# Performance work log

Measured on AMD Instinct MI355X. Metric: run time of the kernel, lower is better.

The kernel has to match this reference:

```python
import jax, jax.numpy as jnp
import numpy as np

B, N, IN_C, OUT_C, H, M, E = 1, 20000, 256, 64, 4, 30, 320000
EPS = 1e-6


def _projection_matrix(m, d, seed=0):
    # NodeFormer create_projection_matrix: stacked transposed-QR blocks, rows
    # rescaled by norms of iid gaussian rows (scaling=0).
    rng = np.random.RandomState(seed)
    blocks = []
    nb_full = m // d
    for _ in range(nb_full):
        q, _ = np.linalg.qr(rng.randn(d, d))
        blocks.append(q.T)
    rem = m - nb_full * d
    if rem > 0:
        q, _ = np.linalg.qr(rng.randn(d, d))
        blocks.append(q.T[:rem])
    final = np.vstack(blocks)
    multiplier = np.linalg.norm(rng.randn(m, d), axis=1)
    return jnp.asarray(multiplier[:, None] * final, dtype=jnp.float32)


def _linear(key, out_f, in_f):
    k1, k2 = jax.random.split(key)
    s = 1.0 / np.sqrt(in_f)
    w = jax.random.uniform(k1, (out_f, in_f), jnp.float32, -s, s)
    b = jax.random.uniform(k2, (out_f,), jnp.float32, -s, s)
    return w, b


def setup_inputs() -> dict:
    key = jax.random.key(0)
    ks = jax.random.split(key, 8)
    Wq_w, Wq_b = _linear(ks[3], H * OUT_C, IN_C)
    Wk_w, Wk_b = _linear(ks[4], H * OUT_C, IN_C)
    Wv_w, Wv_b = _linear(ks[5], H * OUT_C, IN_C)
    Wo_w, Wo_b = _linear(ks[6], OUT_C, H * OUT_C)
    return {
        'z': jax.random.normal(ks[0], (B, N, IN_C), jnp.float32),
        'feat': jax.random.normal(ks[1], (B, N, IN_C), jnp.float32),
        'edge_index': jax.random.randint(ks[2], (2, E), 0, N),
        'tau': jnp.asarray(0.25, jnp.float32),
        'Wq_w': Wq_w, 'Wq_b': Wq_b,
        'Wk_w': Wk_w, 'Wk_b': Wk_b,
        'Wv_w': Wv_w, 'Wv_b': Wv_b,
        'Wo_w': Wo_w, 'Wo_b': Wo_b,
        'b_param': jnp.full((1, H), 0.1, jnp.float32),  # rb_order=1, sigmoid init
        'proj': _projection_matrix(M, OUT_C),
    }


def _softmax_kernel(x, proj, is_query):
    # Performer positive softmax kernel feature map. x: [B,N,H,D] -> [B,N,H,M]
    d = x.shape[-1]
    x = x * (float(d) ** -0.25)
    ratio = 1.0 / jnp.sqrt(jnp.asarray(proj.shape[0], x.dtype))
    xd = jnp.einsum('bnhd,md->bnhm', x, proj)
    diag = 0.5 * jnp.sum(x * x, axis=-1, keepdims=True)
    if is_query:
        mx = jnp.max(xd, axis=-1, keepdims=True)
    else:
        mx = jnp.max(jnp.max(xd, axis=-1, keepdims=True), axis=1, keepdims=True)
    return ratio * (jnp.exp(xd - diag - mx) + EPS)


def reference(z, feat, edge_index, tau, Wq_w, Wq_b, Wk_w, Wk_b, Wv_w, Wv_b,
              Wo_w, Wo_b, b_param, proj):
    Bn, Nn = z.shape[0], z.shape[1]
    q = (feat @ Wq_w.T + Wq_b).reshape(Bn, Nn, H, OUT_C)
    k = (feat @ Wk_w.T + Wk_b).reshape(Bn, Nn, H, OUT_C)
    v = (z @ Wv_w.T + Wv_b).reshape(Bn, Nn, H, OUT_C)

    inv = 1.0 / jnp.sqrt(tau)
    qp = _softmax_kernel(q * inv, proj, True)    # [B,N,H,M]
    kp = _softmax_kernel(k * inv, proj, False)   # [B,N,H,M]

    # Linear (kernelized) attention, O(N*H*M*D)
    kvs = jnp.einsum('bnhm,bnhd->bhmd', kp, v)
    num = jnp.einsum('bnhm,bhmd->bnhd', qp, kvs)
    den = jnp.einsum('bnhm,bhm->bnh', qp, jnp.sum(kp, axis=1))[..., None]
    z_next = num / den                            # [B,N,H,D]

    # Relational bias: GCN-style normalized scatter with per-head scalar weight
    row, col = edge_index[0], edge_index[1]
    d_in = jnp.zeros((Nn,), z.dtype).at[col].add(1.0)
    d_out = jnp.zeros((Nn,), z.dtype).at[row].add(1.0)
    edge_w = jnp.nan_to_num(jnp.sqrt(1.0 / d_in[col]) * jnp.sqrt(1.0 / d_out[row]),
                            nan=0.0, posinf=0.0, neginf=0.0)    # [E]
    msgs = v[:, row] * edge_w[None, :, None, None]              # [B,E,H,D]
    agg = jnp.zeros_like(v).at[:, col].add(msgs)                # [B,N,H,D]
    z_next = z_next + jax.nn.sigmoid(b_param[0])[None, None, :, None] * agg

    out = z_next.reshape(Bn, Nn, H * OUT_C) @ Wo_w.T + Wo_b     # [B,N,OUT_C]
    return out
```

## Files before the change

kernel.cpp:

```cpp
#include <hip/hip_runtime.h>

#define NN 20000
#define EE 320000
#define RATIO_F 0.18257418583505536f
#define EPS_F 1e-6f
#define SCALE_D4 0.35355339059327373f
#define NCH 157

typedef _Float16 f16x8 __attribute__((ext_vector_type(8)));
typedef _Float16 f16x4 __attribute__((ext_vector_type(4)));
typedef float f32x4 __attribute__((ext_vector_type(4)));

__device__ __forceinline__ unsigned fenc(float x) {
  unsigned u = __float_as_uint(x);
  return (u & 0x80000000u) ? ~u : (u | 0x80000000u);
}
__device__ __forceinline__ float fdec(unsigned u) {
  return (u & 0x80000000u) ? __uint_as_float(u & 0x7FFFFFFFu) : __uint_as_float(~u);
}
__device__ __forceinline__ void fma4(float* a, float s, float4 b) {
  a[0] = fmaf(s, b.x, a[0]);
  a[1] = fmaf(s, b.y, a[1]);
  a[2] = fmaf(s, b.z, a[2]);
  a[3] = fmaf(s, b.w, a[3]);
}
__device__ __forceinline__ void gload16(const void* g, void* l) {
  __builtin_amdgcn_global_load_lds(
      (const __attribute__((address_space(1))) unsigned int*)g,
      (__attribute__((address_space(3))) unsigned int*)l, 16, 0, 0);
}

__global__ __launch_bounds__(256)
void k0_build(const float* __restrict__ Wq, const float* __restrict__ Wk,
              const float* __restrict__ Wv, const float* __restrict__ bq,
              const float* __restrict__ bk, const float* __restrict__ bv,
              const float* __restrict__ proj, const float* __restrict__ tau,
              const float* __restrict__ Wo, const int* __restrict__ ei,
              const float* __restrict__ feat, const float* __restrict__ zin,
              _Float16* __restrict__ Wf, float* __restrict__ bbig,
              _Float16* __restrict__ WoFh, _Float16* __restrict__ WoFl,
              int* __restrict__ dini, int* __restrict__ douti,
              _Float16* __restrict__ feath, _Float16* __restrict__ zh16) {
  const int blk = blockIdx.x;
  const int i = threadIdx.x;
  if (blk >= 1401) {
    int cb = blk - 1401;
    const float* src;
    _Float16* dst;
    if (cb < 2500) { src = feat; dst = feath; }
    else           { src = zin;  dst = zh16; cb -= 2500; }
    const size_t off = (size_t)cb * 2048 + i * 8;
    const float4 a = *(const float4*)(src + off);
    const float4 b = *(const float4*)(src + off + 4);
    f16x8 o;
    o[0] = (_Float16)a.x; o[1] = (_Float16)a.y;
    o[2] = (_Float16)a.z; o[3] = (_Float16)a.w;
    o[4] = (_Float16)b.x; o[5] = (_Float16)b.y;
    o[6] = (_Float16)b.z; o[7] = (_Float16)b.w;
    *(f16x8*)(dst + off) = o;
    return;
  }
  if (blk >= 1088) {
    const int q = (blk - 1088) * 256 + i;
    if (q < EE / 4) {
      const int4 r4 = *(const int4*)(ei + q * 4);
      const int4 c4 = *(const int4*)(ei + EE + q * 4);
      atomicAdd(&dini[c4.x], 1); atomicAdd(&dini[c4.y], 1);
      atomicAdd(&dini[c4.z], 1); atomicAdd(&dini[c4.w], 1);
      atomicAdd(&douti[r4.x], 1); atomicAdd(&douti[r4.y], 1);
      atomicAdd(&douti[r4.z], 1); atomicAdd(&douti[r4.w], 1);
    }
    return;
  }
  const int kt = i >> 5, gg = (i >> 3) & 3, j = i & 7;
  if (blk >= 1024) {
    const int col = blk - 1024;
    const float val = Wo[col * 256 + i];
    const int lane = gg * 16 + (col & 15);
    const size_t off = (size_t)((col >> 4) * 8 + kt) * 512 + lane * 8 + j;
    const _Float16 hb = (_Float16)val;
    WoFh[off] = hb;
    WoFl[off] = (_Float16)(val - (float)hb);
    return;
  }
  const int col = blk;
  const float s = rsqrtf(tau[0]) * SCALE_D4;
  float val = 0.f, bias = 0.f;
  if (col < 256) {
    val = Wq[col * 256 + i]; bias = bq[col];
  } else if (col < 512) {
    const int c = col - 256;
    val = Wk[c * 256 + i]; bias = bk[c];
  } else if (col < 768) {
    const int c = col - 512;
    val = Wv[c * 256 + i]; bias = bv[c];
  } else {
    const int rr = col - 768;
    const int grp = rr >> 7;
    const int h = (rr >> 5) & 3, m = rr & 31;
    if (m < 30) {
      const float* W = grp ? Wk : Wq;
      const float* bb = grp ? bk : bq;
      float a = 0.f, ba = 0.f;
#pragma unroll 8
      for (int d = 0; d < 64; ++d) {
        const float pr = proj[m * 64 + d];
        a  = fmaf(pr, W[(h * 64 + d) * 256 + i], a);
        ba = fmaf(pr, bb[h * 64 + d], ba);
      }
      val = s * a; bias = s * ba;
    }
  }
  const int lane = gg * 16 + (col & 15);
  const size_t off = (size_t)((col >> 4) * 8 + kt) * 512 + lane * 8 + j;
  Wf[off] = (_Float16)val;
  if (i == 0) bbig[col] = bias;
}

__device__ __forceinline__ int ct_of(int s, int isv, int h, int y) {
  if (isv) return 32 + (y - 4) * 8 + s;
  if (s < 4)  return h * 4 + s;
  if (s < 8)  return 16 + h * 4 + (s - 4);
  if (s < 10) return 48 + 2 * h + (s - 8);
  return 56 + 2 * h + (s - 10);
}

__global__ __launch_bounds__(512, 4)
void k1_all(const _Float16* __restrict__ feath, const _Float16* __restrict__ zh16,
            const _Float16* __restrict__ Wf, const float* __restrict__ bbig,
            const float* __restrict__ tau,
            _Float16* __restrict__ qph, float* __restrict__ kbuf,
            _Float16* __restrict__ vh, unsigned* __restrict__ kmaxU) {
  __shared__ __align__(16) _Float16 blds[12 * 2048];
  const int t = threadIdx.x;
  const int wid = t >> 6, lane = t & 63;
  const int g = lane >> 4, cl = lane & 15;
  const int y = blockIdx.y;
  const int h = y & 3;
  const int rbase = blockIdx.x * 128 + wid * 16;
  int arow = rbase + cl; if (arow > NN - 1) arow = NN - 1;

  if (y < 4) {
    const _Float16* arp = feath + (size_t)arow * 256;
#pragma unroll
    for (int r = 0; r < 6; ++r) {
      const int idx = r * 4096 + t * 8;
      const int s = idx >> 11, wi = idx & 2047;
      gload16(Wf + (size_t)ct_of(s, 0, h, y) * 4096 + wi, &blds[idx]);
    }
    f16x8 Ah[4];
#pragma unroll
    for (int l = 0; l < 4; ++l)
      Ah[l] = *(const f16x8*)(arp + l * 32 + g * 8);
    __syncthreads();
    f16x8 Ah2[4];
#pragma unroll
    for (int l = 0; l < 4; ++l)
      Ah2[l] = *(const f16x8*)(arp + (l + 4) * 32 + g * 8);
    f32x4 acc[12];
#pragma unroll
    for (int s = 0; s < 12; ++s) acc[s] = (f32x4){0.f, 0.f, 0.f, 0.f};
#pragma unroll
    for (int ktl = 0; ktl < 4; ++ktl) {
#pragma unroll
      for (int s = 0; s < 12; ++s) {
        const f16x8 b = *(const f16x8*)&blds[s * 2048 + ktl * 512 + lane * 8];
        acc[s] = __builtin_amdgcn_mfma_f32_16x16x32_f16(Ah[ktl], b, acc[s], 0, 0, 0);
      }
    }
    __syncthreads();
#pragma unroll
    for (int r = 0; r < 6; ++r) {
      const int idx = r * 4096 + t * 8;
      const int s = idx >> 11, wi = idx & 2047;
      gload16(Wf + (size_t)ct_of(s, 0, h, y) * 4096 + 2048 + wi, &blds[idx]);
    }
    __syncthreads();
#pragma unroll
    for (int ktl = 0; ktl < 4; ++ktl) {
#pragma unroll
      for (int s = 0; s < 12; ++s) {
        const f16x8 b = *(const f16x8*)&blds[s * 2048 + ktl * 512 + lane * 8];
        acc[s] = __builtin_amdgcn_mfma_f32_16x16x32_f16(Ah2[ktl], b, acc[s], 0, 0, 0);
      }
    }
#pragma unroll
    for (int s = 0; s < 12; ++s) {
      const float bb = bbig[ct_of(s, 0, h, y) * 16 + cl];
#pragma unroll
      for (int j = 0; j < 4; ++j) acc[s][j] += bb;
    }
    const float sc = rsqrtf(tau[0]) * SCALE_D4;
    const float h2 = 0.5f * sc * sc;
    float dsq[4], dsk[4];
#pragma unroll
    for (int j = 0; j < 4; ++j) {
      dsq[j] = acc[0][j] * acc[0][j] + acc[1][j] * acc[1][j] +
               acc[2][j] * acc[2][j] + acc[3][j] * acc[3][j];
      dsk[j] = acc[4][j] * acc[4][j] + acc[5][j] * acc[5][j] +
               acc[6][j] * acc[6][j] + acc[7][j] * acc[7][j];
    }
#pragma unroll
    for (int m = 1; m < 16; m <<= 1) {
#pragma unroll
      for (int j = 0; j < 4; ++j) {
        dsq[j] += __shfl_xor(dsq[j], m);
        dsk[j] += __shfl_xor(dsk[j], m);
      }
    }
    {
#pragma unroll
      for (int j = 0; j < 4; ++j) {
        const float x0 = acc[8][j], x1 = acc[9][j];
        float mv = fmaxf(x0, (cl < 14) ? x1 : -3.4e38f);
#pragma unroll
        for (int m = 1; m < 16; m <<= 1) mv = fmaxf(mv, __shfl_xor(mv, m));
        const float dg = h2 * dsq[j];
        const int r = rbase + 4 * g + j;
        if (r < NN) {
          _Float16* dst = qph + (size_t)r * 120 + h * 30;
          dst[cl] = (_Float16)(RATIO_F * (expf(x0 - dg - mv) + EPS_F));
          if (cl < 14)
            dst[16 + cl] = (_Float16)(RATIO_F * (expf(x1 - dg - mv) + EPS_F));
        }
      }
    }
    {
      float wmax = -3.4e38f;
#pragma unroll
      for (int j = 0; j < 4; ++j) {
        const float x0 = acc[10][j], x1 = acc[11][j];
        float mv = fmaxf(x0, (cl < 14) ? x1 : -3.4e38f);
#pragma unroll
        for (int m = 1; m < 16; m <<= 1) mv = fmaxf(mv, __shfl_xor(mv, m));
        wmax = fmaxf(wmax, mv);
        const float dg = h2 * dsk[j];
        const int r = rbase + 4 * g + j;
        if (r < NN) {
          float* dst = kbuf + (size_t)r * 120 + h * 30;
          dst[cl] = x0 - dg;
          if (cl < 14) dst[16 + cl] = x1 - dg;
        }
      }
      wmax = fmaxf(wmax, __shfl_xor(wmax, 16));
      wmax = fmaxf(wmax, __shfl_xor(wmax, 32));
      if (lane == 0) atomicMax(&kmaxU[h], fenc(wmax));
    }
  } else {
    const _Float16* arp = zh16 + (size_t)arow * 256;
#pragma unroll
    for (int r = 0; r < 4; ++r) {
      const int idx = r * 4096 + t * 8;
      const int s = idx >> 11, wi = idx & 2047;
      gload16(Wf + (size_t)ct_of(s, 1, h, y) * 4096 + wi, &blds[idx]);
    }
    f16x8 Ah[4];
#pragma unroll
    for (int l = 0; l < 4; ++l)
      Ah[l] = *(const f16x8*)(arp + l * 32 + g * 8);
    __syncthreads();
    f16x8 Ah2[4];
#pragma unroll
    for (int l = 0; l < 4; ++l)
      Ah2[l] = *(const f16x8*)(arp + (l + 4) * 32 + g * 8);
    f32x4 acc[8];
#pragma unroll
    for (int s = 0; s < 8; ++s) acc[s] = (f32x4){0.f, 0.f, 0.f, 0.f};
#pragma unroll
    for (int ktl = 0; ktl < 4; ++ktl) {
#pragma unroll
      for (int s = 0; s < 8; ++s) {
        const f16x8 b = *(const f16x8*)&blds[s * 2048 + ktl * 512 + lane * 8];
        acc[s] = __builtin_amdgcn_mfma_f32_16x16x32_f16(Ah[ktl], b, acc[s], 0, 0, 0);
      }
    }
    __syncthreads();
#pragma unroll
    for (int r = 0; r < 4; ++r) {
      const int idx = r * 4096 + t * 8;
      const int s = idx >> 11, wi = idx & 2047;
      gload16(Wf + (size_t)ct_of(s, 1, h, y) * 4096 + 2048 + wi, &blds[idx]);
    }
    __syncthreads();
#pragma unroll
    for (int ktl = 0; ktl < 4; ++ktl) {
#pragma unroll
      for (int s = 0; s < 8; ++s) {
        const f16x8 b = *(const f16x8*)&blds[s * 2048 + ktl * 512 + lane * 8];
        acc[s] = __builtin_amdgcn_mfma_f32_16x16x32_f16(Ah2[ktl], b, acc[s], 0, 0, 0);
      }
    }
#pragma unroll
    for (int s = 0; s < 8; ++s) {
      const int ct = ct_of(s, 1, h, y);
      const float bb = bbig[ct * 16 + cl];
      const int colb = (ct - 32) * 16 + cl;
#pragma unroll
      for (int j = 0; j < 4; ++j) {
        const int r = rbase + 4 * g + j;
        if (r < NN) vh[(size_t)r * 256 + colb] = (_Float16)(acc[s][j] + bb);
      }
    }
  }
}

__global__ __launch_bounds__(256)
void k3_kvs(const float* __restrict__ kbr, const _Float16* __restrict__ vh,
            const unsigned* __restrict__ kmaxU, float* __restrict__ partial) {
  __shared__ float kpch[128 * 32];
  __shared__ float vch[128 * 68];
  const int h = blockIdx.y;
  const int n0 = blockIdx.x * 128;
  const int cnt = min(128, NN - n0);
  const int t = threadIdx.x;
  const float mx = fdec(kmaxU[h]);
  const int m = t >> 3, dg = t & 7, d0 = dg * 8;
#pragma unroll
  for (int l = 0; l < 15; ++l) {
    const int flat = l * 256 + t;
    const int nl = flat / 30, mm = flat - nl * 30;
    kpch[nl * 32 + mm] = (nl < cnt)
        ? RATIO_F * (expf(kbr[(size_t)(n0 + nl) * 120 + h * 30 + mm] - mx) + EPS_F)
        : 0.f;
  }
#pragma unroll
  for (int l = 0; l < 8; ++l) {
    const int f4 = l * 256 + t;
    const int nl = f4 >> 4, dd = (f4 & 15) * 4;
    float4 vv = make_float4(0.f, 0.f, 0.f, 0.f);
    if (nl < cnt) {
      f16x4 u = *(const f16x4*)(vh + (size_t)(n0 + nl) * 256 + h * 64 + dd);
      vv = make_float4((float)u[0], (float)u[1], (float)u[2], (float)u[3]);
    }
    *(float4*)&vch[nl * 68 + dd] = vv;
  }
  __syncthreads();
  float acc[8] = {0, 0, 0, 0, 0, 0, 0, 0};
  float asum = 0.f;
  const int ms = (m < 30) ? m : 0;
  for (int nl = 0; nl < cnt; ++nl) {
    const float kv = kpch[nl * 32 + ms];
    const float4 va = *(const float4*)&vch[nl * 68 + d0];
    const float4 vb = *(const float4*)&vch[nl * 68 + d0 + 4];
    fma4(&acc[0], kv, va);
    fma4(&acc[4], kv, vb);
    asum += kv;
  }
  if (m < 30) {
    float* dst = partial + ((size_t)blockIdx.y * NCH + blockIdx.x) * 1952 + m * 64 + d0;
#pragma unroll
    for (int j = 0; j < 8; ++j) dst[j] = acc[j];
    if (dg == 0)
      partial[((size_t)blockIdx.y * NCH + blockIdx.x) * 1952 + 1920 + m] = asum;
  }
}

__global__ __launch_bounds__(256)
void k3b_reduce(const float* __restrict__ partial, float* __restrict__ kvs,
                float* __restrict__ ksum) {
  const int idx = blockIdx.x * 256 + threadIdx.x;
  if (idx >= 4 * 1952) return;
  const int h = idx / 1952, q = idx - h * 1952;
  float s = 0.f;
  for (int c = 0; c < NCH; ++c)
    s += partial[((size_t)h * NCH + c) * 1952 + q];
  if (q < 1920) kvs[h * 1920 + q] = s;
  else if (q < 1950) ksum[h * 30 + (q - 1920)] = s;
}

__global__ __launch_bounds__(256)
void k4_attn(const _Float16* __restrict__ qph, const float* __restrict__ kvs,
             const float* __restrict__ ksum, const _Float16* __restrict__ aggh,
             const float* __restrict__ bp, _Float16* __restrict__ zh) {
  __shared__ float kvsl[120 * 68];
  __shared__ float ksl[120];
  __shared__ float qpl[32 * 120];
  const int t = threadIdx.x;
  const int n0 = blockIdx.x * 32;
#pragma unroll
  for (int l = 0; l < 30; ++l) {
    const int f = l * 256 + t;
    const int hm = f >> 6, d = f & 63;
    kvsl[hm * 68 + d] = kvs[f];
  }
  if (t < 120) ksl[t] = ksum[t];
#pragma unroll
  for (int l = 0; l < 15; ++l) {
    const int f = l * 256 + t;
    qpl[f] = (float)qph[(size_t)n0 * 120 + f];
  }
  __syncthreads();
  const int nl = t >> 3, dg = t & 7, d0 = dg * 8;
  const float* qrow = &qpl[nl * 120];
  float den[4] = {0, 0, 0, 0};
  for (int m = 0; m < 30; ++m) {
#pragma unroll
    for (int hh = 0; hh < 4; ++hh) den[hh] = fmaf(qrow[hh * 30 + m], ksl[hh * 30 + m], den[hh]);
  }
  float acc[4][8] = {};
  for (int m = 0; m < 30; ++m) {
#pragma unroll
    for (int hh = 0; hh < 4; ++hh) {
      const float qv = qrow[hh * 30 + m];
      const float* kr = &kvsl[(hh * 30 + m) * 68 + d0];
      const float4 ka = *(const float4*)kr;
      const float4 kb = *(const float4*)(kr + 4);
      fma4(&acc[hh][0], qv, ka);
      fma4(&acc[hh][4], qv, kb);
    }
  }
  const size_t n = n0 + nl;
#pragma unroll
  for (int hh = 0; hh < 4; ++hh) {
    const float inv = 1.0f / den[hh];
    const float sg = 1.f / (1.f + expf(-bp[hh]));
    const f16x8 ag = *(const f16x8*)(aggh + n * 256 + hh * 64 + d0);
    f16x8 o;
#pragma unroll
    for (int jj = 0; jj < 8; ++jj)
      o[jj] = (_Float16)(acc[hh][jj] * inv + sg * (float)ag[jj]);
    *(f16x8*)(zh + n * 256 + hh * 64 + d0) = o;
  }
}

__global__ __launch_bounds__(1024)
void k6a_scan(const int* __restrict__ cnt, int* __restrict__ off) {
  __shared__ int s[1024];
  const int t = threadIdx.x;
  int4 v[5];
  int sum = 0;
  const int4* p4 = (const int4*)(cnt + t * 20);
#pragma unroll
  for (int i = 0; i < 5; ++i) {
    v[i] = p4[i];
    sum += v[i].x + v[i].y + v[i].z + v[i].w;
  }
  s[t] = sum;
  __syncthreads();
  for (int o = 1; o < 1024; o <<= 1) {
    const int add = (t >= o) ? s[t - o] : 0;
    __syncthreads();
    s[t] += add;
    __syncthreads();
  }
  int run = (t == 0) ? 0 : s[t - 1];
  if (t == 0) off[0] = 0;
  const int base = t * 20;
#pragma unroll
  for (int i = 0; i < 5; ++i) {
    const int vals[4] = {v[i].x, v[i].y, v[i].z, v[i].w};
#pragma unroll
    for (int j = 0; j < 4; ++j) {
      const int idx = base + i * 4 + j;
      if (idx < NN) { run += vals[j]; off[idx + 1] = run; }
    }
  }
}

__global__ __launch_bounds__(256)
void k6bc(const int* __restrict__ ei, const int* __restrict__ coff,
          int* __restrict__ cursor, int* __restrict__ crow,
          const int* __restrict__ douti, float* __restrict__ rw) {
  const int b = blockIdx.x;
  if (b < EE / 256) {
    const int e = b * 256 + threadIdx.x;
    const int r = ei[e], c = ei[EE + e];
    const int pos = atomicAdd(&cursor[c], 1);
    crow[coff[c] + pos] = r;
  } else {
    const int n = (b - EE / 256) * 256 + threadIdx.x;
    if (n < NN) rw[n] = rsqrtf((float)douti[n]);
  }
}

__global__ __launch_bounds__(256)
void k7g_gather(const int* __restrict__ coff, const int* __restrict__ crow,
                const float* __restrict__ rw, const _Float16* __restrict__ vh,
                _Float16* __restrict__ aggh) {
  const int node = blockIdx.x * 4 + (threadIdx.x >> 6);
  const int lane = threadIdx.x & 63;
  const int o0 = coff[node], o1 = coff[node + 1];
  float a0 = 0.f, a1 = 0.f, a2 = 0.f, a3 = 0.f;
  if (o1 > o0) {
    int e = o0;
    for (; e + 16 <= o1; e += 16) {
      int rr[16];
#pragma unroll
      for (int u = 0; u < 16; ++u) rr[u] = crow[e + u];
      float ww[16];
#pragma unroll
      for (int u = 0; u < 16; ++u) ww[u] = rw[rr[u]];
#pragma unroll
      for (int u = 0; u < 16; ++u) {
        const f16x4 vv = *(const f16x4*)(vh + (size_t)rr[u] * 256 + lane * 4);
        a0 = fmaf(ww[u], (float)vv[0], a0);
        a1 = fmaf(ww[u], (float)vv[1], a1);
        a2 = fmaf(ww[u], (float)vv[2], a2);
        a3 = fmaf(ww[u], (float)vv[3], a3);
      }
    }
    for (; e + 4 <= o1; e += 4) {
      int rr[4];
#pragma unroll
      for (int u = 0; u < 4; ++u) rr[u] = crow[e + u];
      float ww[4];
#pragma unroll
      for (int u = 0; u < 4; ++u) ww[u] = rw[rr[u]];
#pragma unroll
      for (int u = 0; u < 4; ++u) {
        const f16x4 vv = *(const f16x4*)(vh + (size_t)rr[u] * 256 + lane * 4);
        a0 = fmaf(ww[u], (float)vv[0], a0);
        a1 = fmaf(ww[u], (float)vv[1], a1);
        a2 = fmaf(ww[u], (float)vv[2], a2);
        a3 = fmaf(ww[u], (float)vv[3], a3);
      }
    }
    for (; e < o1; ++e) {
      const int r = crow[e];
      const float wr = rw[r];
      const f16x4 vv = *(const f16x4*)(vh + (size_t)r * 256 + lane * 4);
      a0 = fmaf(wr, (float)vv[0], a0);
      a1 = fmaf(wr, (float)vv[1], a1);
      a2 = fmaf(wr, (float)vv[2], a2);
      a3 = fmaf(wr, (float)vv[3], a3);
    }
    const float rin = rsqrtf((float)(o1 - o0));
    a0 *= rin; a1 *= rin; a2 *= rin; a3 *= rin;
  }
  f16x4 st;
  st[0] = (_Float16)a0; st[1] = (_Float16)a1;
  st[2] = (_Float16)a2; st[3] = (_Float16)a3;
  *(f16x4*)(aggh + (size_t)node * 256 + lane * 4) = st;
}

__global__ __launch_bounds__(512, 4)
void k8m_out(const _Float16* __restrict__ zh, const _Float16* __restrict__ WoFh,
             const _Float16* __restrict__ WoFl, const float* __restrict__ bo,
             float* __restrict__ out) {
  __shared__ __align__(16) _Float16 blds[8 * 4096];
  const int t = threadIdx.x;
  const int wid = t >> 6, lane = t & 63;
  const int g = lane >> 4, cl = lane & 15;
  const int rt = wid >> 2, ct = wid & 3;
  const int rbase = blockIdx.x * 32 + rt * 16;
  int arow = rbase + cl; if (arow > NN - 1) arow = NN - 1;
#pragma unroll
  for (int s = 0; s < 4; ++s) {
    gload16(WoFh + (size_t)s * 4096 + t * 8, &blds[(s * 512 + t) * 8]);
    gload16(WoFl + (size_t)s * 4096 + t * 8, &blds[((s + 4) * 512 + t) * 8]);
  }
  const _Float16* zr = zh + (size_t)arow * 256;
  f16x8 Ah[8];
#pragma unroll
  for (int kt = 0; kt < 8; ++kt)
    Ah[kt] = *(const f16x8*)(zr + kt * 32 + g * 8);
  __syncthreads();
  f32x4 acc = {0.f, 0.f, 0.f, 0.f};
#pragma unroll
  for (int kt = 0; kt < 8; ++kt) {
    const f16x8 bh = *(const f16x8*)&blds[ct * 4096 + kt * 512 + lane * 8];
    const f16x8 bl = *(const f16x8*)&blds[(ct + 4) * 4096 + kt * 512 + lane * 8];
    acc = __builtin_amdgcn_mfma_f32_16x16x32_f16(Ah[kt], bh, acc, 0, 0, 0);
    acc = __builtin_amdgcn_mfma_f32_16x16x32_f16(Ah[kt], bl, acc, 0, 0, 0);
  }
  const float bb = bo[ct * 16 + cl];
#pragma unroll
  for (int j = 0; j < 4; ++j) {
    const int r = rbase + 4 * g + j;
    if (r < NN) out[(size_t)r * 64 + ct * 16 + cl] = acc[j] + bb;
  }
}

extern "C" void kernel_launch(void* const* d_in, const int* in_sizes, int n_in,
                              void* d_out, int out_size, void* d_ws, size_t ws_size,
                              hipStream_t stream) {
  (void)in_sizes; (void)n_in; (void)out_size; (void)ws_size;
  const float* z    = (const float*)d_in[0];
  const float* feat = (const float*)d_in[1];
  const int*   ei   = (const int*)d_in[2];
  const float* tau  = (const float*)d_in[3];
  const float* Wq_w = (const float*)d_in[4];
  const float* Wq_b = (const float*)d_in[5];
  const float* Wk_w = (const float*)d_in[6];
  const float* Wk_b = (const float*)d_in[7];
  const float* Wv_w = (const float*)d_in[8];
  const float* Wv_b = (const float*)d_in[9];
  const float* Wo_w = (const float*)d_in[10];
  const float* Wo_b = (const float*)d_in[11];
  const float* bp   = (const float*)d_in[12];
  const float* proj = (const float*)d_in[13];
  float* out = (float*)d_out;

  char* p = (char*)d_ws;
  auto alloc = [&](size_t bytes) { char* r = p; p += (bytes + 255) & ~(size_t)255; return r; };
  _Float16* Wf    = (_Float16*)alloc((size_t)256 * 1024 * 2);
  _Float16* WoFh  = (_Float16*)alloc((size_t)64 * 256 * 2);
  _Float16* WoFl  = (_Float16*)alloc((size_t)64 * 256 * 2);
  float*    bbig  = (float*)alloc(1024 * 4);
  _Float16* feath = (_Float16*)alloc((size_t)NN * 256 * 2);
  _Float16* zh16  = (_Float16*)alloc((size_t)NN * 256 * 2);
  _Float16* vh    = (_Float16*)alloc((size_t)NN * 256 * 2);
  _Float16* aggh  = (_Float16*)alloc((size_t)NN * 256 * 2);
  _Float16* qph   = (_Float16*)alloc((size_t)NN * 120 * 2);
  float*    kbuf  = (float*)alloc((size_t)NN * 120 * 4);
  _Float16* zh    = (_Float16*)alloc((size_t)NN * 256 * 2);
  float*    partial = (float*)alloc((size_t)4 * NCH * 1952 * 4);
  float*    kvs   = (float*)alloc(7680 * 4);
  float*    ksum  = (float*)alloc(120 * 4);
  float*    rw    = (float*)alloc((size_t)NN * 4);
  char* z0 = p;
  unsigned* kmaxU = (unsigned*)alloc(16);
  int*      dini  = (int*)alloc((size_t)20480 * 4);
  int*      douti = (int*)alloc((size_t)NN * 4);
  int*      cursor= (int*)alloc((size_t)NN * 4);
  char* z1 = p;
  int*      coff  = (int*)alloc((size_t)(NN + 1) * 4);
  int*      crow  = (int*)alloc((size_t)EE * 4);

  hipMemsetAsync(z0, 0, (size_t)(z1 - z0), stream);

  k0_build<<<1401 + 5000, 256, 0, stream>>>(
      Wq_w, Wk_w, Wv_w, Wq_b, Wk_b, Wv_b, proj, tau, Wo_w, ei, feat, z,
      Wf, bbig, WoFh, WoFl, dini, douti, feath, zh16);
  k6a_scan<<<1, 1024, 0, stream>>>(dini, coff);
  k6bc<<<EE / 256 + (NN + 255) / 256, 256, 0, stream>>>(ei, coff, cursor, crow,
                                                        douti, rw);
  k1_all<<<dim3(157, 6), 512, 0, stream>>>(feath, zh16, Wf, bbig, tau, qph, kbuf, vh, kmaxU);
  k7g_gather<<<NN / 4, 256, 0, stream>>>(coff, crow, rw, vh, aggh);
  k3_kvs<<<dim3(NCH, 4), 256, 0, stream>>>(kbuf, vh, kmaxU, partial);
  k3b_reduce<<<(4 * 1952 + 255) / 256, 256, 0, stream>>>(partial, kvs, ksum);
  k4_attn<<<NN / 32, 256, 0, stream>>>(qph, kvs, ksum, aggh, bp, zh);
  k8m_out<<<628, 512, 0, stream>>>(zh, WoFh, WoFl, Wo_b, out);
}
```

Before: 254.5 us.

## Merge CSR fill into projection kernel, fuse gather with kvs reduce, store k logits in fp16

The CSR row fill and degree-weight kernel is folded into the projection kernel as extra blocks, and the edge gather is merged with the kvs partial reduction into one launch. Two kernel launches go away and the independent work can overlap. The key logits buffer is now stored as fp16 instead of fp32, which halves its write and read traffic but loses precision before the exp. Merging the CSR fill into the projection grid also changes the dependency: before the gather, only block-level ordering within one launch exists, so the fill and gather are still kept in separate kernels.

```diff
diff --git a/kernel.cpp b/kernel.cpp
--- a/kernel.cpp
+++ b/kernel.cpp
@@ -126,18 +126,34 @@
 }
 
 __global__ __launch_bounds__(512, 4)
-void k1_all(const _Float16* __restrict__ feath, const _Float16* __restrict__ zh16,
-            const _Float16* __restrict__ Wf, const float* __restrict__ bbig,
-            const float* __restrict__ tau,
-            _Float16* __restrict__ qph, float* __restrict__ kbuf,
-            _Float16* __restrict__ vh, unsigned* __restrict__ kmaxU) {
+void k1m(const _Float16* __restrict__ feath, const _Float16* __restrict__ zh16,
+         const _Float16* __restrict__ Wf, const float* __restrict__ bbig,
+         const float* __restrict__ tau,
+         _Float16* __restrict__ qph, _Float16* __restrict__ kbufh,
+         _Float16* __restrict__ vh, unsigned* __restrict__ kmaxU,
+         const int* __restrict__ ei, const int* __restrict__ coff,
+         int* __restrict__ cursor, int* __restrict__ crow,
+         const int* __restrict__ douti, float* __restrict__ rw) {
   __shared__ __align__(16) _Float16 blds[12 * 2048];
+  const int blk = blockIdx.x;
   const int t = threadIdx.x;
+  if (blk >= 1567) {
+    const int n = (blk - 1567) * 512 + t;
+    if (n < NN) rw[n] = rsqrtf((float)douti[n]);
+    return;
+  }
+  if (blk >= 942) {
+    const int e = (blk - 942) * 512 + t;
+    const int r = ei[e], c = ei[EE + e];
+    const int pos = atomicAdd(&cursor[c], 1);
+    crow[coff[c] + pos] = r;
+    return;
+  }
+  const int y = blk / 157;
+  const int h = y & 3;
   const int wid = t >> 6, lane = t & 63;
   const int g = lane >> 4, cl = lane & 15;
-  const int y = blockIdx.y;
-  const int h = y & 3;
-  const int rbase = blockIdx.x * 128 + wid * 16;
+  const int rbase = (blk - y * 157) * 128 + wid * 16;
   int arow = rbase + cl; if (arow > NN - 1) arow = NN - 1;
 
   if (y < 4) {
@@ -237,9 +253,9 @@
         const float dg = h2 * dsk[j];
         const int r = rbase + 4 * g + j;
         if (r < NN) {
-          float* dst = kbuf + (size_t)r * 120 + h * 30;
-          dst[cl] = x0 - dg;
-          if (cl < 14) dst[16 + cl] = x1 - dg;
+          _Float16* dst = kbufh + (size_t)r * 120 + h * 30;
+          dst[cl] = (_Float16)(x0 - dg);
+          if (cl < 14) dst[16 + cl] = (_Float16)(x1 - dg);
         }
       }
       wmax = fmaxf(wmax, __shfl_xor(wmax, 16));
@@ -305,7 +321,7 @@
 }
 
 __global__ __launch_bounds__(256)
-void k3_kvs(const float* __restrict__ kbr, const _Float16* __restrict__ vh,
+void k3_kvs(const _Float16* __restrict__ kbr, const _Float16* __restrict__ vh,
             const unsigned* __restrict__ kmaxU, float* __restrict__ partial) {
   __shared__ float kpch[128 * 32];
   __shared__ float vch[128 * 68];
@@ -320,7 +336,7 @@
     const int flat = l * 256 + t;
     const int nl = flat / 30, mm = flat - nl * 30;
     kpch[nl * 32 + mm] = (nl < cnt)
-        ? RATIO_F * (expf(kbr[(size_t)(n0 + nl) * 120 + h * 30 + mm] - mx) + EPS_F)
+        ? RATIO_F * (expf((float)kbr[(size_t)(n0 + nl) * 120 + h * 30 + mm] - mx) + EPS_F)
         : 0.f;
   }
 #pragma unroll
@@ -356,16 +372,76 @@
 }
 
 __global__ __launch_bounds__(256)
-void k3b_reduce(const float* __restrict__ partial, float* __restrict__ kvs,
-                float* __restrict__ ksum) {
-  const int idx = blockIdx.x * 256 + threadIdx.x;
-  if (idx >= 4 * 1952) return;
-  const int h = idx / 1952, q = idx - h * 1952;
-  float s = 0.f;
-  for (int c = 0; c < NCH; ++c)
-    s += partial[((size_t)h * NCH + c) * 1952 + q];
-  if (q < 1920) kvs[h * 1920 + q] = s;
-  else if (q < 1950) ksum[h * 30 + (q - 1920)] = s;
+void k7g3b(const int* __restrict__ coff, const int* __restrict__ crow,
+           const float* __restrict__ rw, const _Float16* __restrict__ vh,
+           _Float16* __restrict__ aggh, const float* __restrict__ partial,
+           float* __restrict__ kvs, float* __restrict__ ksum) {
+  const int blk = blockIdx.x;
+  if (blk >= 5000) {
+    const int idx = (blk - 5000) * 256 + threadIdx.x;
+    if (idx >= 4 * 1952) return;
+    const int h = idx / 1952, q = idx - h * 1952;
+    float s = 0.f;
+    for (int c = 0; c < NCH; ++c)
+      s += partial[((size_t)h * NCH + c) * 1952 + q];
+    if (q < 1920) kvs[h * 1920 + q] = s;
+    else if (q < 1950) ksum[h * 30 + (q - 1920)] = s;
+    return;
+  }
+  const int node = blk * 4 + (threadIdx.x >> 6);
+  const int lane = threadIdx.x & 63;
+  const int o0 = coff[node], o1 = coff[node + 1];
+  float a0 = 0.f, a1 = 0.f, a2 = 0.f, a3 = 0.f;
+  if (o1 > o0) {
+    int e = o0;
+    for (; e + 16 <= o1; e += 16) {
+      int rr[16];
+#pragma unroll
+      for (int u = 0; u < 16; ++u) rr[u] = crow[e + u];
+      float ww[16];
+#pragma unroll
+      for (int u = 0; u < 16; ++u) ww[u] = rw[rr[u]];
+#pragma unroll
+      for (int u = 0; u < 16; ++u) {
+        const f16x4 vv = *(const f16x4*)(vh + (size_t)rr[u] * 256 + lane * 4);
+        a0 = fmaf(ww[u], (float)vv[0], a0);
+        a1 = fmaf(ww[u], (float)vv[1], a1);
+        a2 = fmaf(ww[u], (float)vv[2], a2);
+        a3 = fmaf(ww[u], (float)vv[3], a3);
+      }
+    }
+    for (; e + 4 <= o1; e += 4) {
+      int rr[4];
+#pragma unroll
+      for (int u = 0; u < 4; ++u) rr[u] = crow[e + u];
+      float ww[4];
+#pragma unroll
+      for (int u = 0; u < 4; ++u) ww[u] = rw[rr[u]];
+#pragma unroll
+      for (int u = 0; u < 4; ++u) {
+        const f16x4 vv = *(const f16x4*)(vh + (size_t)rr[u] * 256 + lane * 4);
+        a0 = fmaf(ww[u], (float)vv[0], a0);
+        a1 = fmaf(ww[u], (float)vv[1], a1);
+        a2 = fmaf(ww[u], (float)vv[2], a2);
+        a3 = fmaf(ww[u], (float)vv[3], a3);
+      }
+    }
+    for (; e < o1; ++e) {
+      const int r = crow[e];
+      const float wr = rw[r];
+      const f16x4 vv = *(const f16x4*)(vh + (size_t)r * 256 + lane * 4);
+      a0 = fmaf(wr, (float)vv[0], a0);
+      a1 = fmaf(wr, (float)vv[1], a1);
+      a2 = fmaf(wr, (float)vv[2], a2);
+      a3 = fmaf(wr, (float)vv[3], a3);
+    }
+    const float rin = rsqrtf((float)(o1 - o0));
+    a0 *= rin; a1 *= rin; a2 *= rin; a3 *= rin;
+  }
+  f16x4 st;
+  st[0] = (_Float16)a0; st[1] = (_Float16)a1;
+  st[2] = (_Float16)a2; st[3] = (_Float16)a3;
+  *(f16x4*)(aggh + (size_t)node * 256 + lane * 4) = st;
 }
 
 __global__ __launch_bounds__(256)
@@ -455,82 +531,6 @@
       if (idx < NN) { run += vals[j]; off[idx + 1] = run; }
     }
   }
-}
-
-__global__ __launch_bounds__(256)
-void k6bc(const int* __restrict__ ei, const int* __restrict__ coff,
-          int* __restrict__ cursor, int* __restrict__ crow,
-          const int* __restrict__ douti, float* __restrict__ rw) {
-  const int b = blockIdx.x;
-  if (b < EE / 256) {
-    const int e = b * 256 + threadIdx.x;
-    const int r = ei[e], c = ei[EE + e];
-    const int pos = atomicAdd(&cursor[c], 1);
-    crow[coff[c] + pos] = r;
-  } else {
-    const int n = (b - EE / 256) * 256 + threadIdx.x;
-    if (n < NN) rw[n] = rsqrtf((float)douti[n]);
-  }
-}
-
-__global__ __launch_bounds__(256)
-void k7g_gather(const int* __restrict__ coff, const int* __restrict__ crow,
-                const float* __restrict__ rw, const _Float16* __restrict__ vh,
-                _Float16* __restrict__ aggh) {
-  const int node = blockIdx.x * 4 + (threadIdx.x >> 6);
-  const int lane = threadIdx.x & 63;
-  const int o0 = coff[node], o1 = coff[node + 1];
-  float a0 = 0.f, a1 = 0.f, a2 = 0.f, a3 = 0.f;
-  if (o1 > o0) {
-    int e = o0;
-    for (; e + 16 <= o1; e += 16) {
-      int rr[16];
-#pragma unroll
-      for (int u = 0; u < 16; ++u) rr[u] = crow[e + u];
-      float ww[16];
-#pragma unroll
-      for (int u = 0; u < 16; ++u) ww[u] = rw[rr[u]];
-#pragma unroll
-      for (int u = 0; u < 16; ++u) {
-        const f16x4 vv = *(const f16x4*)(vh + (size_t)rr[u] * 256 + lane * 4);
-        a0 = fmaf(ww[u], (float)vv[0], a0);
-        a1 = fmaf(ww[u], (float)vv[1], a1);
-        a2 = fmaf(ww[u], (float)vv[2], a2);
-        a3 = fmaf(ww[u], (float)vv[3], a3);
-      }
-    }
-    for (; e + 4 <= o1; e += 4) {
-      int rr[4];
-#pragma unroll
-      for (int u = 0; u < 4; ++u) rr[u] = crow[e + u];
-      float ww[4];
-#pragma unroll
-      for (int u = 0; u < 4; ++u) ww[u] = rw[rr[u]];
-#pragma unroll
-      for (int u = 0; u < 4; ++u) {
-        const f16x4 vv = *(const f16x4*)(vh + (size_t)rr[u] * 256 + lane * 4);
-        a0 = fmaf(ww[u], (float)vv[0], a0);
-        a1 = fmaf(ww[u], (float)vv[1], a1);
-        a2 = fmaf(ww[u], (float)vv[2], a2);
-        a3 = fmaf(ww[u], (float)vv[3], a3);
-      }
-    }
-    for (; e < o1; ++e) {
-      const int r = crow[e];
-      const float wr = rw[r];
-      const f16x4 vv = *(const f16x4*)(vh + (size_t)r * 256 + lane * 4);
-      a0 = fmaf(wr, (float)vv[0], a0);
-      a1 = fmaf(wr, (float)vv[1], a1);
-      a2 = fmaf(wr, (float)vv[2], a2);
-      a3 = fmaf(wr, (float)vv[3], a3);
-    }
-    const float rin = rsqrtf((float)(o1 - o0));
-    a0 *= rin; a1 *= rin; a2 *= rin; a3 *= rin;
-  }
-  f16x4 st;
-  st[0] = (_Float16)a0; st[1] = (_Float16)a1;
-  st[2] = (_Float16)a2; st[3] = (_Float16)a3;
-  *(f16x4*)(aggh + (size_t)node * 256 + lane * 4) = st;
 }
 
 __global__ __launch_bounds__(512, 4)
@@ -602,7 +602,7 @@
   _Float16* vh    = (_Float16*)alloc((size_t)NN * 256 * 2);
   _Float16* aggh  = (_Float16*)alloc((size_t)NN * 256 * 2);
   _Float16* qph   = (_Float16*)alloc((size_t)NN * 120 * 2);
-  float*    kbuf  = (float*)alloc((size_t)NN * 120 * 4);
+  _Float16* kbufh = (_Float16*)alloc((size_t)NN * 120 * 2);
   _Float16* zh    = (_Float16*)alloc((size_t)NN * 256 * 2);
   float*    partial = (float*)alloc((size_t)4 * NCH * 1952 * 4);
   float*    kvs   = (float*)alloc(7680 * 4);
@@ -623,12 +623,11 @@
       Wq_w, Wk_w, Wv_w, Wq_b, Wk_b, Wv_b, proj, tau, Wo_w, ei, feat, z,
       Wf, bbig, WoFh, WoFl, dini, douti, feath, zh16);
   k6a_scan<<<1, 1024, 0, stream>>>(dini, coff);
-  k6bc<<<EE / 256 + (NN + 255) / 256, 256, 0, stream>>>(ei, coff, cursor, crow,
-                                                        douti, rw);
-  k1_all<<<dim3(157, 6), 512, 0, stream>>>(feath, zh16, Wf, bbig, tau, qph, kbuf, vh, kmaxU);
-  k7g_gather<<<NN / 4, 256, 0, stream>>>(coff, crow, rw, vh, aggh);
-  k3_kvs<<<dim3(NCH, 4), 256, 0, stream>>>(kbuf, vh, kmaxU, partial);
-  k3b_reduce<<<(4 * 1952 + 255) / 256, 256, 0, stream>>>(partial, kvs, ksum);
+  k1m<<<1607, 512, 0, stream>>>(feath, zh16, Wf, bbig, tau, qph, kbufh, vh,
+                                kmaxU, ei, coff, cursor, crow, douti, rw);
+  k3_kvs<<<dim3(NCH, 4), 256, 0, stream>>>(kbufh, vh, kmaxU, partial);
+  k7g3b<<<5000 + (4 * 1952 + 255) / 256, 256, 0, stream>>>(
+      coff, crow, rw, vh, aggh, partial, kvs, ksum);
   k4_attn<<<NN / 32, 256, 0, stream>>>(qph, kvs, ksum, aggh, bp, zh);
   k8m_out<<<628, 512, 0, stream>>>(zh, WoFh, WoFl, Wo_b, out);
 }
```

Result: faster. 233.2 us (-8.4%).
